# Kernel tuning notes

Measured on AMD Instinct MI355X. Metric: run time of the kernel, lower is better.

The kernel has to match this reference:

```python
import jax, jax.numpy as jnp
import numpy as np

N, E, G = 50000, 200000, 512
F_N, F_E, H, L = 64, 16, 32, 3
EPS = 1e-5


def setup_inputs() -> dict:
    key = jax.random.key(0)
    ks = jax.random.split(key, 20)
    s = 0.1
    inp = {
        'x': jax.random.normal(ks[0], (N, F_N), jnp.float32),
        'edge_attr': jax.random.normal(ks[1], (E, F_E), jnp.float32),
        'W_node': jax.random.normal(ks[2], (F_N, H), jnp.float32) * s,
        'b_node': jnp.zeros((H,), jnp.float32),
        'W_edge': jax.random.normal(ks[3], (F_E, 2 * F_E), jnp.float32) * s,
        'b_edge': jnp.zeros((2 * F_E,), jnp.float32),
        'W_nn': jax.random.normal(ks[4], (L, 2 * F_E, H * H), jnp.float32) * s,
        'b_nn': jnp.zeros((L, H * H), jnp.float32),
        'W_root': jax.random.normal(ks[5], (L, H, H), jnp.float32) * s,
        'b_conv': jnp.zeros((L, H), jnp.float32),
        'gamma': jnp.ones((L, H), jnp.float32),
        'beta': jnp.zeros((L, H), jnp.float32),
        'W2': jax.random.normal(ks[6], (H, H // 2), jnp.float32) * s,
        'b2': jnp.zeros((H // 2,), jnp.float32),
        'W3': jax.random.normal(ks[7], (H // 2, 1), jnp.float32) * s,
        'b3': jnp.zeros((1,), jnp.float32),
        'edge_index': jax.random.randint(ks[8], (2, E), 0, N, jnp.int32),
        'batch': jnp.sort(jax.random.randint(ks[9], (N,), 0, G, jnp.int32)),
    }
    return inp


def reference(x, edge_attr, W_node, b_node, W_edge, b_edge, W_nn, b_nn,
              W_root, b_conv, gamma, beta, W2, b2, W3, b3, edge_index, batch):
    src, dst = edge_index[0], edge_index[1]
    h = x @ W_node + b_node                      # [N,H] node_emb
    ea = edge_attr @ W_edge + b_edge             # [E,2*F_E] edge_emb
    for l in range(L):
        # NNConv: per-edge weight matrix from edge features
        We = (ea @ W_nn[l] + b_nn[l]).reshape(E, H, H)   # [E,H,H]
        m = jnp.einsum('ei,eio->eo', h[src], We)         # gather + per-edge transform
        agg = jax.ops.segment_sum(m, dst, num_segments=N)  # scatter-add aggregation
        h = h @ W_root[l] + agg + b_conv[l]
        # BatchNorm (batch statistics over nodes) + ReLU
        mu = h.mean(axis=0)
        var = h.var(axis=0)
        h = jax.nn.relu((h - mu) * jax.lax.rsqrt(var + EPS) * gamma[l] + beta[l])
    # global mean pool over graphs
    cnt = jax.ops.segment_sum(jnp.ones((N,), h.dtype), batch, num_segments=G)
    gsum = jax.ops.segment_sum(h, batch, num_segments=G)
    gx = gsum / jnp.maximum(cnt, 1.0)[:, None]   # [G,H]
    # head: lin2 -> relu -> (dropout=identity at eval) -> lin3
    hh = jax.nn.relu(gx @ W2 + b2)
    return hh @ W3 + b3                          # [G,1]
```

## Files before the change

### kernel.cpp

```cpp
#include <hip/hip_runtime.h>

#define NN 50000
#define NE 200000
#define NG 512
#define NB 6250
#define FN 64
#define FE 16
#define FE2 32
#define H 32
#define NL 3
#define EPSV 1e-5f

__global__ void k_prep(const float* __restrict__ Wnn, const float* __restrict__ We,
                       const float* __restrict__ be, const float* __restrict__ Bnn,
                       float* __restrict__ V2, float* __restrict__ M,
                       const int* __restrict__ src, const int* __restrict__ batch,
                       int* __restrict__ degB, float* __restrict__ cnt,
                       const float* __restrict__ x, const float* __restrict__ Wn,
                       const float* __restrict__ bno, float* __restrict__ h,
                       float* __restrict__ agg) {
    __shared__ float smem[2048];
    int t = threadIdx.x;
    int b = blockIdx.x;
    if (b < 96) {
        int l = b >> 5, i = b & 31;
        float* sWnn = smem;
        float* sWe  = smem + 1024;
        for (int j = t; j < 1024; j += 256)
            sWnn[j] = Wnn[((size_t)(l * 32 + (j >> 5))) * 1024 + i * 32 + (j & 31)];
        for (int j = t; j < 512; j += 256) sWe[j] = We[j];
        __syncthreads();
#pragma unroll
        for (int cc = 0; cc < 2; cc++) {
            int c = 2 * t + cc;
            int f = c >> 5, o = c & 31;
            float v = 0.f;
#pragma unroll
            for (int k = 0; k < 32; k++) v += sWe[f * 32 + k] * sWnn[k * 32 + o];
            V2[(size_t)(l * 32 + i) * 512 + c] = v;
        }
        if (t < 32) {
            float m = Bnn[(size_t)l * 1024 + i * 32 + t];
            for (int k = 0; k < 32; k++) m += be[k] * sWnn[k * 32 + t];
            M[l * 1024 + i * 32 + t] = m;
        }
    } else if (b < 878) {
        for (int j = t; j < FN * H; j += 256) smem[j] = Wn[j];
        __syncthreads();
        int n0 = (b - 96) * 64;
        int node8 = t >> 5, o = t & 31;
        for (int r = 0; r < 8; r++) {
            int n = n0 + r * 8 + node8;
            if (n < NN) {
                const float* xr = x + (size_t)n * FN;
                float acc = bno[o];
#pragma unroll 16
                for (int i = 0; i < FN; i++) acc += xr[i] * smem[i * H + o];
                size_t idx = (size_t)n * H + o;
                h[idx] = acc;
                agg[idx] = 0.f;
            }
        }
    } else {
        int e = (b - 878) * 256 + t;
        if (e < NE) atomicAdd(&degB[src[e] >> 3], 1);
        if (e < NN) atomicAdd(&cnt[batch[e]], 1.f);
    }
}

__global__ void k_scanB(const int* __restrict__ degB, int* __restrict__ rowptrB,
                        int* __restrict__ cursorB) {
    __shared__ int ssum[1024];
    int t = threadIdx.x;
    int loc[7];
    int base = t * 7;
    int s = 0;
#pragma unroll
    for (int i = 0; i < 7; i++) {
        int idx = base + i;
        loc[i] = (idx < NB) ? degB[idx] : 0;
        s += loc[i];
    }
    ssum[t] = s;
    for (int off = 1; off < 1024; off <<= 1) {
        __syncthreads();
        int tv = (t >= off) ? ssum[t - off] : 0;
        __syncthreads();
        ssum[t] += tv;
    }
    __syncthreads();
    int run = ssum[t] - s;
#pragma unroll
    for (int i = 0; i < 7; i++) {
        int idx = base + i;
        if (idx < NB) { rowptrB[idx] = run; cursorB[idx] = run; run += loc[i]; }
    }
    if (t == 1023) rowptrB[NB] = ssum[1023];
}

__global__ void k_fill(const int* __restrict__ src, int* __restrict__ cursorB,
                       int* __restrict__ eid) {
    int e = blockIdx.x * 256 + threadIdx.x;
    if (e >= NE) return;
    int p = atomicAdd(&cursorB[src[e] >> 3], 1);
    eid[p] = e;
}

__global__ __launch_bounds__(256, 4) void k_conv(
    const float* __restrict__ h0, const float* __restrict__ eattr,
    const float* __restrict__ V2l, const float* __restrict__ Ml,
    const int* __restrict__ rowptrB, const int* __restrict__ eid,
    const int* __restrict__ src, const int* __restrict__ dst,
    float* __restrict__ agg, float* __restrict__ z,
    const float* __restrict__ statsPrev, float* __restrict__ statsZero,
    const float* __restrict__ gm, const float* __restrict__ bt,
    const float* __restrict__ Wr, const float* __restrict__ bc, int first) {
    __shared__ __align__(16) float sU[8][512];
    __shared__ __align__(16) float shh[8][32];
    __shared__ __align__(16) float su[8][32];
    __shared__ __align__(16) float sea[4][2][32];
    int t = threadIdx.x;
    int nb0 = blockIdx.x * 8;
    if (blockIdx.x == 0 && t < 64) statsZero[t] = 0.f;

    {
        int node = t >> 5, o = t & 31;
        size_t idx = (size_t)(nb0 + node) * H + o;
        float hv;
        if (first) {
            hv = h0[idx];
        } else {
            const float invn = 1.0f / (float)NN;
            float mu = statsPrev[o] * invn;
            float var = statsPrev[32 + o] * invn - mu * mu;
            float v = (z[idx] - mu) * rsqrtf(var + EPSV) * gm[o] + bt[o];
            hv = v > 0.f ? v : 0.f;
        }
        shh[node][o] = hv;
        __builtin_amdgcn_wave_barrier();
        float a = bc[o], bacc = 0.f;
#pragma unroll
        for (int i = 0; i < H; i++) {
            float hh = shh[node][i];
            a += hh * Wr[i * H + o];
            bacc += hh * Ml[i * H + o];
        }
        z[idx] = a;
        su[node][o] = bacc;
    }
    __syncthreads();

    {
        const float* vp = V2l + 2 * t;
        float2 acc[8];
#pragma unroll
        for (int n = 0; n < 8; n++) acc[n] = make_float2(0.f, 0.f);
#pragma unroll
        for (int i4 = 0; i4 < 8; i4++) {
            float2 v0 = *(const float2*)(vp + (size_t)(i4 * 4 + 0) * 512);
            float2 v1 = *(const float2*)(vp + (size_t)(i4 * 4 + 1) * 512);
            float2 v2 = *(const float2*)(vp + (size_t)(i4 * 4 + 2) * 512);
            float2 v3 = *(const float2*)(vp + (size_t)(i4 * 4 + 3) * 512);
#pragma unroll
            for (int n = 0; n < 8; n++) {
                float4 hv = *(const float4*)&shh[n][i4 * 4];
                acc[n].x += hv.x * v0.x + hv.y * v1.x + hv.z * v2.x + hv.w * v3.x;
                acc[n].y += hv.x * v0.y + hv.y * v1.y + hv.z * v2.y + hv.w * v3.y;
            }
        }
#pragma unroll
        for (int n = 0; n < 8; n++)
            *(float2*)&sU[n][2 * t] = acc[n];
    }
    __syncthreads();

    int E0 = rowptrB[blockIdx.x], E1 = rowptrB[blockIdx.x + 1];
    int w = t >> 6;
    int lane = t & 63;
    int hw = lane >> 5;
    int o = lane & 31;
    int buf = 0;
    for (int jb = E0 + 2 * w; jb < E1; jb += 8, buf ^= 1) {
        int j = jb + hw;
        bool act = (j < E1);
        int sn = 0, d = 0;
        if (act) {
            int e = eid[j];
            sn = src[e] - nb0;
            d = dst[e];
            if (o < 16) sea[w][buf][hw * 16 + o] = eattr[(size_t)e * FE + o];
        }
        __builtin_amdgcn_wave_barrier();
        if (act) {
            const float* sef = &sea[w][buf][hw * 16];
            float m = su[sn][o];
            const float* tp = &sU[sn][0];
#pragma unroll
            for (int f4 = 0; f4 < 4; f4++) {
                float4 se = *(const float4*)&sef[f4 * 4];
                m += se.x * tp[(f4 * 4 + 0) * 32 + o];
                m += se.y * tp[(f4 * 4 + 1) * 32 + o];
                m += se.z * tp[(f4 * 4 + 2) * 32 + o];
                m += se.w * tp[(f4 * 4 + 3) * 32 + o];
            }
            atomicAdd(&agg[(size_t)d * H + o], m);
        }
        __builtin_amdgcn_wave_barrier();
    }
}

__global__ void k_add_stats(float* __restrict__ z, float* __restrict__ agg,
                            float* __restrict__ stats) {
    __shared__ float red[256];
    int t = threadIdx.x;
    float s = 0.f, s2 = 0.f;
    for (size_t idx = (size_t)blockIdx.x * 256 + t; idx < (size_t)NN * H;
         idx += (size_t)gridDim.x * 256) {
        float v = z[idx] + agg[idx];
        z[idx] = v;
        agg[idx] = 0.f;
        s += v;
        s2 += v * v;
    }
    red[t] = s;
    __syncthreads();
    for (int st = 128; st >= 32; st >>= 1) {
        if (t < st) red[t] += red[t + st];
        __syncthreads();
    }
    if (t < 32) atomicAdd(&stats[t], red[t]);
    __syncthreads();
    red[t] = s2;
    __syncthreads();
    for (int st = 128; st >= 32; st >>= 1) {
        if (t < st) red[t] += red[t + st];
        __syncthreads();
    }
    if (t < 32) atomicAdd(&stats[32 + t], red[t]);
}

__global__ void k_bn_pool(const float* __restrict__ z, const float* __restrict__ stats,
                          const float* __restrict__ gm, const float* __restrict__ bt,
                          const int* __restrict__ batch, float* __restrict__ gsum) {
    int idx = blockIdx.x * 256 + threadIdx.x;
    if (idx >= NN * H) return;
    int n = idx >> 5, o = idx & 31;
    const float invn = 1.0f / (float)NN;
    float mu = stats[o] * invn;
    float var = stats[32 + o] * invn - mu * mu;
    float v = (z[idx] - mu) * rsqrtf(var + EPSV) * gm[o] + bt[o];
    v = v > 0.f ? v : 0.f;
    atomicAdd(&gsum[(size_t)batch[n] * H + o], v);
}

__global__ void k_head(const float* __restrict__ gsum, const float* __restrict__ cnt,
                       const float* __restrict__ W2, const float* __restrict__ b2,
                       const float* __restrict__ W3, const float* __restrict__ b3,
                       float* __restrict__ out) {
    __shared__ float sW2[H * 16];
    __shared__ float sW3[16];
    __shared__ float sb2[16];
    int t = threadIdx.x;
    for (int j = t; j < H * 16; j += 256) sW2[j] = W2[j];
    if (t < 16) { sW3[t] = W3[t]; sb2[t] = b2[t]; }
    __syncthreads();
    int g = blockIdx.x * 256 + t;
    if (g >= NG) return;
    float inv = 1.0f / fmaxf(cnt[g], 1.0f);
    float gx[H];
#pragma unroll
    for (int i = 0; i < H; i++) gx[i] = gsum[g * H + i] * inv;
    float o3 = b3[0];
#pragma unroll
    for (int j = 0; j < 16; j++) {
        float hh = sb2[j];
#pragma unroll
        for (int i = 0; i < H; i++) hh += gx[i] * sW2[i * 16 + j];
        hh = hh > 0.f ? hh : 0.f;
        o3 += hh * sW3[j];
    }
    out[g] = o3;
}

extern "C" void kernel_launch(void* const* d_in, const int* in_sizes, int n_in,
                              void* d_out, int out_size, void* d_ws, size_t ws_size,
                              hipStream_t stream) {
    const float* x      = (const float*)d_in[0];
    const float* eattr  = (const float*)d_in[1];
    const float* W_node = (const float*)d_in[2];
    const float* b_node = (const float*)d_in[3];
    const float* W_edge = (const float*)d_in[4];
    const float* b_edge = (const float*)d_in[5];
    const float* W_nn   = (const float*)d_in[6];
    const float* b_nn   = (const float*)d_in[7];
    const float* W_root = (const float*)d_in[8];
    const float* b_conv = (const float*)d_in[9];
    const float* gamma  = (const float*)d_in[10];
    const float* beta   = (const float*)d_in[11];
    const float* W2     = (const float*)d_in[12];
    const float* b2     = (const float*)d_in[13];
    const float* W3     = (const float*)d_in[14];
    const float* b3     = (const float*)d_in[15];
    const int* eidx     = (const int*)d_in[16];
    const int* batch    = (const int*)d_in[17];
    const int* src = eidx;
    const int* dst = eidx + NE;
    float* out = (float*)d_out;

    const size_t NNH = (size_t)NN * H;
    float* ws = (float*)d_ws;
    float* h      = ws;
    float* z      = h + NNH;
    float* agg    = z + NNH;
    float* stats  = agg + NNH;
    float* V2     = stats + 128;
    float* M      = V2 + (size_t)NL * 32 * 512;
    int*   degB   = (int*)(M + NL * 1024);
    float* gsum   = (float*)(degB + NB);
    float* cnt    = gsum + (size_t)NG * H;
    int*   rowptrB = (int*)(cnt + NG);
    int*   cursorB = rowptrB + NB + 1;
    int*   eid    = cursorB + NB;

    hipMemsetAsync(degB, 0, (NB + NG * H + NG) * sizeof(int), stream);

    k_prep<<<96 + 782 + 782, 256, 0, stream>>>(
        W_nn, W_edge, b_edge, b_nn, V2, M, src, batch, degB, cnt,
        x, W_node, b_node, h, agg);
    k_scanB<<<1, 1024, 0, stream>>>(degB, rowptrB, cursorB);
    k_fill<<<(NE + 255) / 256, 256, 0, stream>>>(src, cursorB, eid);

    for (int l = 0; l < NL; l++) {
        float* statsCur  = stats + (l & 1) * 64;
        float* statsPrev = stats + ((l + 1) & 1) * 64;
        int lp = (l > 0) ? (l - 1) : 0;
        k_conv<<<NB, 256, 0, stream>>>(h, eattr, V2 + (size_t)l * 32 * 512,
                                       M + (size_t)l * 1024,
                                       rowptrB, eid, src, dst, agg, z,
                                       statsPrev, statsCur,
                                       gamma + lp * H, beta + lp * H,
                                       W_root + (size_t)l * H * H, b_conv + l * H,
                                       l == 0 ? 1 : 0);
        k_add_stats<<<512, 256, 0, stream>>>(z, agg, statsCur);
    }

    k_bn_pool<<<NB, 256, 0, stream>>>(z, stats + ((NL - 1) & 1) * 64,
                                      gamma + (NL - 1) * H, beta + (NL - 1) * H,
                                      batch, gsum);
    k_head<<<2, 256, 0, stream>>>(gsum, cnt, W2, b2, W3, b3, out);
}
```

Before: 357.1 us.

## Pre-permute edge attributes and packed src/dst into CSR order for conv

Result: slower. 372.5 us (+4.3%).

```diff
diff --git a/kernel.cpp b/kernel.cpp
--- a/kernel.cpp
+++ b/kernel.cpp
@@ -6,7 +6,6 @@
 #define NB 6250
 #define FN 64
 #define FE 16
-#define FE2 32
 #define H 32
 #define NL 3
 #define EPSV 1e-5f
@@ -98,19 +97,25 @@
     if (t == 1023) rowptrB[NB] = ssum[1023];
 }
 
-__global__ void k_fill(const int* __restrict__ src, int* __restrict__ cursorB,
-                       int* __restrict__ eid) {
+__global__ void k_fill(const int* __restrict__ src, const int* __restrict__ dst,
+                       const float* __restrict__ eattr, int* __restrict__ cursorB,
+                       unsigned* __restrict__ sdR, float* __restrict__ eaR) {
     int e = blockIdx.x * 256 + threadIdx.x;
     if (e >= NE) return;
-    int p = atomicAdd(&cursorB[src[e] >> 3], 1);
-    eid[p] = e;
+    int s = src[e];
+    int p = atomicAdd(&cursorB[s >> 3], 1);
+    sdR[p] = ((unsigned)dst[e] << 3) | (unsigned)(s & 7);
+    const float4* q = (const float4*)(eattr + (size_t)e * FE);
+    float4* r = (float4*)(eaR + (size_t)p * FE);
+    float4 q0 = q[0], q1 = q[1], q2 = q[2], q3 = q[3];
+    r[0] = q0; r[1] = q1; r[2] = q2; r[3] = q3;
 }
 
 __global__ __launch_bounds__(256, 4) void k_conv(
-    const float* __restrict__ h0, const float* __restrict__ eattr,
+    const float* __restrict__ h0, const unsigned* __restrict__ sdR,
+    const float* __restrict__ eaR,
     const float* __restrict__ V2l, const float* __restrict__ Ml,
-    const int* __restrict__ rowptrB, const int* __restrict__ eid,
-    const int* __restrict__ src, const int* __restrict__ dst,
+    const int* __restrict__ rowptrB,
     float* __restrict__ agg, float* __restrict__ z,
     const float* __restrict__ statsPrev, float* __restrict__ statsZero,
     const float* __restrict__ gm, const float* __restrict__ bt,
@@ -118,7 +123,6 @@
     __shared__ __align__(16) float sU[8][512];
     __shared__ __align__(16) float shh[8][32];
     __shared__ __align__(16) float su[8][32];
-    __shared__ __align__(16) float sea[4][2][32];
     int t = threadIdx.x;
     int nb0 = blockIdx.x * 8;
     if (blockIdx.x == 0 && t < 64) statsZero[t] = 0.f;
@@ -179,33 +183,53 @@
     int lane = t & 63;
     int hw = lane >> 5;
     int o = lane & 31;
-    int buf = 0;
-    for (int jb = E0 + 2 * w; jb < E1; jb += 8, buf ^= 1) {
-        int j = jb + hw;
-        bool act = (j < E1);
-        int sn = 0, d = 0;
-        if (act) {
-            int e = eid[j];
-            sn = src[e] - nb0;
-            d = dst[e];
-            if (o < 16) sea[w][buf][hw * 16 + o] = eattr[(size_t)e * FE + o];
-        }
-        __builtin_amdgcn_wave_barrier();
-        if (act) {
-            const float* sef = &sea[w][buf][hw * 16];
+    for (int jb = E0 + 4 * w; jb < E1; jb += 16) {
+        int ja = jb + 2 * hw;
+        bool a0 = (ja < E1);
+        bool a1 = (ja + 1 < E1);
+        unsigned sd0 = 0, sd1 = 0;
+        float4 e00 = make_float4(0.f, 0.f, 0.f, 0.f), e01 = e00, e02 = e00, e03 = e00;
+        float4 e10 = e00, e11 = e00, e12 = e00, e13 = e00;
+        if (a0) {
+            sd0 = sdR[ja];
+            const float4* p0 = (const float4*)(eaR + (size_t)ja * FE);
+            e00 = p0[0]; e01 = p0[1]; e02 = p0[2]; e03 = p0[3];
+        }
+        if (a1) {
+            sd1 = sdR[ja + 1];
+            const float4* p1 = (const float4*)(eaR + (size_t)(ja + 1) * FE);
+            e10 = p1[0]; e11 = p1[1]; e12 = p1[2]; e13 = p1[3];
+        }
+        if (a0) {
+            int sn = sd0 & 7;
+            unsigned d = sd0 >> 3;
+            const float* tp = &sU[sn][0];
             float m = su[sn][o];
+            m += e00.x * tp[0 * 32 + o] + e00.y * tp[1 * 32 + o]
+               + e00.z * tp[2 * 32 + o] + e00.w * tp[3 * 32 + o];
+            m += e01.x * tp[4 * 32 + o] + e01.y * tp[5 * 32 + o]
+               + e01.z * tp[6 * 32 + o] + e01.w * tp[7 * 32 + o];
+            m += e02.x * tp[8 * 32 + o] + e02.y * tp[9 * 32 + o]
+               + e02.z * tp[10 * 32 + o] + e02.w * tp[11 * 32 + o];
+            m += e03.x * tp[12 * 32 + o] + e03.y * tp[13 * 32 + o]
+               + e03.z * tp[14 * 32 + o] + e03.w * tp[15 * 32 + o];
+            atomicAdd(&agg[(size_t)d * H + o], m);
+        }
+        if (a1) {
+            int sn = sd1 & 7;
+            unsigned d = sd1 >> 3;
             const float* tp = &sU[sn][0];
-#pragma unroll
-            for (int f4 = 0; f4 < 4; f4++) {
-                float4 se = *(const float4*)&sef[f4 * 4];
-                m += se.x * tp[(f4 * 4 + 0) * 32 + o];
-                m += se.y * tp[(f4 * 4 + 1) * 32 + o];
-                m += se.z * tp[(f4 * 4 + 2) * 32 + o];
-                m += se.w * tp[(f4 * 4 + 3) * 32 + o];
-            }
+            float m = su[sn][o];
+            m += e10.x * tp[0 * 32 + o] + e10.y * tp[1 * 32 + o]
+               + e10.z * tp[2 * 32 + o] + e10.w * tp[3 * 32 + o];
+            m += e11.x * tp[4 * 32 + o] + e11.y * tp[5 * 32 + o]
+               + e11.z * tp[6 * 32 + o] + e11.w * tp[7 * 32 + o];
+            m += e12.x * tp[8 * 32 + o] + e12.y * tp[9 * 32 + o]
+               + e12.z * tp[10 * 32 + o] + e12.w * tp[11 * 32 + o];
+            m += e13.x * tp[12 * 32 + o] + e13.y * tp[13 * 32 + o]
+               + e13.z * tp[14 * 32 + o] + e13.w * tp[15 * 32 + o];
             atomicAdd(&agg[(size_t)d * H + o], m);
         }
-        __builtin_amdgcn_wave_barrier();
     }
 }
 
@@ -320,7 +344,8 @@
     float* cnt    = gsum + (size_t)NG * H;
     int*   rowptrB = (int*)(cnt + NG);
     int*   cursorB = rowptrB + NB + 1;
-    int*   eid    = cursorB + NB;
+    unsigned* sdR = (unsigned*)(cursorB + NB);
+    float* eaR    = (float*)(sdR + NE);
 
     hipMemsetAsync(degB, 0, (NB + NG * H + NG) * sizeof(int), stream);
 
@@ -328,15 +353,15 @@
         W_nn, W_edge, b_edge, b_nn, V2, M, src, batch, degB, cnt,
         x, W_node, b_node, h, agg);
     k_scanB<<<1, 1024, 0, stream>>>(degB, rowptrB, cursorB);
-    k_fill<<<(NE + 255) / 256, 256, 0, stream>>>(src, cursorB, eid);
+    k_fill<<<(NE + 255) / 256, 256, 0, stream>>>(src, dst, eattr, cursorB, sdR, eaR);
 
     for (int l = 0; l < NL; l++) {
         float* statsCur  = stats + (l & 1) * 64;
         float* statsPrev = stats + ((l + 1) & 1) * 64;
         int lp = (l > 0) ? (l - 1) : 0;
-        k_conv<<<NB, 256, 0, stream>>>(h, eattr, V2 + (size_t)l * 32 * 512,
+        k_conv<<<NB, 256, 0, stream>>>(h, sdR, eaR, V2 + (size_t)l * 32 * 512,
                                        M + (size_t)l * 1024,
-                                       rowptrB, eid, src, dst, agg, z,
+                                       rowptrB, agg, z,
                                        statsPrev, statsCur,
                                        gamma + lp * H, beta + lp * H,
                                        W_root + (size_t)l * H * H, b_conv + l * H,
@@ -344,8 +369,8 @@
         k_add_stats<<<512, 256, 0, stream>>>(z, agg, statsCur);
     }
 
-    k_bn_pool<<<NB, 256, 0, stream>>>(z, stats + ((NL - 1) & 1) * 64,
-                                      gamma + (NL - 1) * H, beta + (NL - 1) * H,
-                                      batch, gsum);
+    k_bn_pool<<<(NN * H + 255) / 256, 256, 0, stream>>>(
+        z, stats + ((NL - 1) & 1) * 64,
+        gamma + (NL - 1) * H, beta + (NL - 1) * H, batch, gsum);
     k_head<<<2, 256, 0, stream>>>(gsum, cnt, W2, b2, W3, b3, out);
 }
```
